# Kernel optimization log

Measured on AMD Instinct MI355X. Metric: run time of the kernel, lower is better.

Reference implementation:

```python
import jax, jax.numpy as jnp
import numpy as np

N_EMBD = 1024
N_HEAD = 16

def _lin_params(key, fan_in, fan_out):
    kw, kb = jax.random.split(key)
    bound = 1.0 / np.sqrt(fan_in)
    W = jax.random.uniform(kw, (fan_in, fan_out), minval=-bound, maxval=bound, dtype=jnp.float32)
    b = jax.random.uniform(kb, (fan_out,), minval=-bound, maxval=bound, dtype=jnp.float32)
    return W, b

def setup_inputs() -> dict:
    key = jax.random.key(0)
    ks = jax.random.split(key, 6)
    x = jax.random.normal(ks[0], (2, 2048, N_EMBD), dtype=jnp.float32)
    W_attn, b_attn = _lin_params(ks[1], N_EMBD, 3 * N_EMBD)
    W_proj, b_proj = _lin_params(ks[2], N_EMBD, N_EMBD)
    W_fc, b_fc = _lin_params(ks[3], N_EMBD, 4 * N_EMBD)
    W_fc2, b_fc2 = _lin_params(ks[4], 4 * N_EMBD, N_EMBD)
    ln1_g = jnp.ones((N_EMBD,), jnp.float32); ln1_b = jnp.zeros((N_EMBD,), jnp.float32)
    ln2_g = jnp.ones((N_EMBD,), jnp.float32); ln2_b = jnp.zeros((N_EMBD,), jnp.float32)
    return {"x": x, "W_attn": W_attn, "b_attn": b_attn, "W_proj": W_proj, "b_proj": b_proj,
            "W_fc": W_fc, "b_fc": b_fc, "W_fc2": W_fc2, "b_fc2": b_fc2,
            "ln1_g": ln1_g, "ln1_b": ln1_b, "ln2_g": ln2_g, "ln2_b": ln2_b}

def _layernorm(x, g, b, eps=1e-5):
    mu = jnp.mean(x, axis=-1, keepdims=True)
    var = jnp.var(x, axis=-1, keepdims=True)
    return (x - mu) * jax.lax.rsqrt(var + eps) * g + b

def _attention(x, W_attn, b_attn, W_proj, b_proj):
    B, T, C = x.shape
    hd = C // N_HEAD
    qkv = x @ W_attn + b_attn                      # [B,T,3C]
    q, k, v = jnp.split(qkv, 3, axis=-1)
    # [B,T,C] -> [B,H,T,hd]
    q = q.reshape(B, T, N_HEAD, hd).transpose(0, 2, 1, 3)
    k = k.reshape(B, T, N_HEAD, hd).transpose(0, 2, 1, 3)
    v = v.reshape(B, T, N_HEAD, hd).transpose(0, 2, 1, 3)
    att = jnp.einsum('bhqd,bhkd->bhqk', q, k) * (1.0 / np.sqrt(hd))
    causal = jnp.tril(jnp.ones((T, T), bool))
    att = jnp.where(causal[None, None], att, -jnp.inf)
    att = jax.nn.softmax(att, axis=-1)
    y = jnp.einsum('bhqk,bhkd->bhqd', att, v)      # [B,H,T,hd]
    y = y.transpose(0, 2, 1, 3).reshape(B, T, C)
    return y @ W_proj + b_proj

def _mlp(x, W_fc, b_fc, W_fc2, b_fc2):
    h = jax.nn.gelu(x @ W_fc + b_fc, approximate=False)
    return h @ W_fc2 + b_fc2

def reference(x, W_attn, b_attn, W_proj, b_proj, W_fc, b_fc, W_fc2, b_fc2,
              ln1_g, ln1_b, ln2_g, ln2_b):
    x = x + _attention(_layernorm(x, ln1_g, ln1_b), W_attn, b_attn, W_proj, b_proj)
    x = x + _mlp(_layernorm(x, ln2_g, ln2_b), W_fc, b_fc, W_fc2, b_fc2)
    return x
```

## Files before the change

### kernel.cpp

```cpp
#include <hip/hip_runtime.h>
#include <cstdint>
#include <cstddef>


typedef unsigned short u16;
typedef short bf16x8 __attribute__((ext_vector_type(8)));
typedef float f32x4 __attribute__((ext_vector_type(4)));

#define C_EMBD 1024
#define T_SEQ  2048
#define N_BATCH 2
#define N_HEADS 16
#define HEAD_D 64
#define M_TOK  4096

__device__ __forceinline__ u16 f2b(float f) {
  union { float f; unsigned u; } v; v.f = f;
  unsigned r = (v.u + 0x7fffu + ((v.u >> 16) & 1u)) >> 16;
  return (u16)r;
}
__device__ __forceinline__ float b2f(u16 u) {
  union { unsigned u; float f; } v; v.u = ((unsigned)u) << 16;
  return v.f;
}
__device__ __forceinline__ void load_lds16(const void* g, void* l) {
  __builtin_amdgcn_global_load_lds(
      (const __attribute__((address_space(1))) void*)g,
      (__attribute__((address_space(3))) void*)l, 16, 0, 0);
}
__device__ __forceinline__ float gelu_fast(float x) {
  const float p = x * __builtin_fmaf(0.044715f * x, x, 1.0f);
  const float t = __builtin_amdgcn_exp2f(2.3021859215f * p);
  return x * t * __builtin_amdgcn_rcpf(t + 1.0f);
}

__global__ __launch_bounds__(256) void transpose_cast(
    const float* __restrict__ W, u16* __restrict__ Wt, int K, int N) {
  __shared__ float tile[32][33];
  const int n0 = blockIdx.x * 32, k0 = blockIdx.y * 32;
  const int tx = threadIdx.x & 31, ty = threadIdx.x >> 5;
#pragma unroll
  for (int i = 0; i < 32; i += 8)
    tile[ty + i][tx] = W[(size_t)(k0 + ty + i) * N + n0 + tx];
  __syncthreads();
#pragma unroll
  for (int i = 0; i < 32; i += 8)
    Wt[(size_t)(n0 + ty + i) * K + k0 + tx] = f2b(tile[tx][ty + i]);
}

__global__ __launch_bounds__(256) void ln_cast(
    const float* __restrict__ X, const float* __restrict__ g,
    const float* __restrict__ b, u16* __restrict__ Y) {
  const int row = blockIdx.x;
  const int tid = threadIdx.x;
  const float4 v = ((const float4*)(X + (size_t)row * C_EMBD))[tid];
  float s = v.x + v.y + v.z + v.w;
  float ss = v.x * v.x + v.y * v.y + v.z * v.z + v.w * v.w;
#pragma unroll
  for (int off = 32; off > 0; off >>= 1) {
    s += __shfl_down(s, off, 64);
    ss += __shfl_down(ss, off, 64);
  }
  __shared__ float red[8];
  __shared__ float stats[2];
  const int wave = tid >> 6, lane = tid & 63;
  if (lane == 0) { red[wave] = s; red[4 + wave] = ss; }
  __syncthreads();
  if (tid == 0) {
    float S = red[0] + red[1] + red[2] + red[3];
    float SS = red[4] + red[5] + red[6] + red[7];
    float mu = S * (1.0f / C_EMBD);
    float var = SS * (1.0f / C_EMBD) - mu * mu;
    stats[0] = mu;
    stats[1] = rsqrtf(var + 1e-5f);
  }
  __syncthreads();
  const float mu = stats[0], rs = stats[1];
  const float4 gv = ((const float4*)g)[tid];
  const float4 bv = ((const float4*)b)[tid];
  ushort4 o;
  o.x = f2b((v.x - mu) * rs * gv.x + bv.x);
  o.y = f2b((v.y - mu) * rs * gv.y + bv.y);
  o.z = f2b((v.z - mu) * rs * gv.z + bv.z);
  o.w = f2b((v.w - mu) * rs * gv.w + bv.w);
  ((ushort4*)(Y + (size_t)row * C_EMBD))[tid] = o;
}

enum { EPI_BF16 = 0, EPI_GELU_BF16 = 2, EPI_PART = 3 };

template <int EPI, int SPLIT>
__global__ __launch_bounds__(256) void gemm_bt(
    const u16* __restrict__ A, const u16* __restrict__ Bt,
    const float* __restrict__ bias,
    void* __restrict__ Cout, void* __restrict__ Cout2, int M, int N, int K) {
  __shared__ u16 As[128 * 64];
  __shared__ u16 Bs[128 * 64];
  const int tid = threadIdx.x;
  const int wave = tid >> 6, lane = tid & 63;
  const int quad = lane >> 4, l16 = lane & 15;
  const int sw = l16 & 7;
  const int m0 = blockIdx.y * 128, n0 = blockIdx.x * 128;
  const int wm = (wave >> 1) * 64, wn = (wave & 1) * 64;

  f32x4 acc[4][4] = {};

  const int kTiles = (K >> 6) / SPLIT;
  const int kt0 = (SPLIT == 2) ? (int)blockIdx.z * kTiles : 0;
  for (int kt = kt0; kt < kt0 + kTiles; ++kt) {
    const int k0 = kt << 6;
#pragma unroll
    for (int i = 0; i < 4; ++i) {
      const int c = tid + i * 256;
      const int row = c >> 3, gc = ((c & 7) ^ (row & 7)) * 8;
      load_lds16(A + (size_t)(m0 + row) * K + k0 + gc, &As[c * 8]);
    }
#pragma unroll
    for (int i = 0; i < 4; ++i) {
      const int c = tid + i * 256;
      const int row = c >> 3, gc = ((c & 7) ^ (row & 7)) * 8;
      load_lds16(Bt + (size_t)(n0 + row) * K + k0 + gc, &Bs[c * 8]);
    }
    __syncthreads();
#pragma unroll
    for (int ks = 0; ks < 2; ++ks) {
      bf16x8 aF[4], bF[4];
#pragma unroll
      for (int t = 0; t < 4; ++t) {
        aF[t] = *(const bf16x8*)
            &As[(wm + t * 16 + l16) * 64 + (((ks * 4 + quad) ^ sw) * 8)];
        bF[t] = *(const bf16x8*)
            &Bs[(wn + t * 16 + l16) * 64 + (((ks * 4 + quad) ^ sw) * 8)];
      }
#pragma unroll
      for (int tm = 0; tm < 4; ++tm)
#pragma unroll
        for (int tn = 0; tn < 4; ++tn)
          acc[tm][tn] = __builtin_amdgcn_mfma_f32_16x16x32_bf16(
              bF[tn], aF[tm], acc[tm][tn], 0, 0, 0);
    }
    __syncthreads();
  }

  float* Pz = (float*)((SPLIT == 2 && blockIdx.z == 1) ? Cout2 : Cout);
#pragma unroll
  for (int tm = 0; tm < 4; ++tm) {
    const int row = m0 + wm + tm * 16 + l16;
#pragma unroll
    for (int tn = 0; tn < 4; ++tn) {
      const int col = n0 + wn + tn * 16 + quad * 4;
      if constexpr (EPI == EPI_PART) {
        *(float4*)&Pz[(size_t)row * N + col] = *(float4*)&acc[tm][tn];
      } else {
        const float4 bz = *(const float4*)&bias[col];
        float v0 = acc[tm][tn][0] + bz.x, v1 = acc[tm][tn][1] + bz.y;
        float v2 = acc[tm][tn][2] + bz.z, v3 = acc[tm][tn][3] + bz.w;
        if constexpr (EPI == EPI_GELU_BF16) {
          v0 = gelu_fast(v0); v1 = gelu_fast(v1);
          v2 = gelu_fast(v2); v3 = gelu_fast(v3);
        }
        ushort4 o;
        o.x = f2b(v0); o.y = f2b(v1); o.z = f2b(v2); o.w = f2b(v3);
        *(ushort4*)&((u16*)Cout)[(size_t)row * N + col] = o;
      }
    }
  }
}

__global__ __launch_bounds__(256) void reduce_add(
    const float* __restrict__ P0, const float* __restrict__ P1,
    const float* __restrict__ bias, const float* __restrict__ res,
    float* __restrict__ out) {
  const int idx = blockIdx.x * 256 + threadIdx.x;
  const float4 a = ((const float4*)P0)[idx];
  const float4 b = ((const float4*)P1)[idx];
  const float4 c = ((const float4*)res)[idx];
  const float4 g = ((const float4*)bias)[idx & 255];
  float4 o;
  o.x = a.x + b.x + c.x + g.x;
  o.y = a.y + b.y + c.y + g.y;
  o.z = a.z + b.z + c.z + g.z;
  o.w = a.w + b.w + c.w + g.w;
  ((float4*)out)[idx] = o;
}

#define Q_SCALE 0.18033688011112042f

__global__ __launch_bounds__(256) void reorder_qkv(
    const u16* __restrict__ qkv, u16* __restrict__ Q, u16* __restrict__ Kb,
    u16* __restrict__ Vt) {
  const int bh = blockIdx.y, tb = blockIdx.x;
  const int b = bh >> 4, h = bh & 15;
  const size_t row0 = (size_t)b * T_SEQ + tb * 64;
  __shared__ u16 vt[64][68];
  const int tid = threadIdx.x;
#pragma unroll
  for (int i = 0; i < 4; ++i) {
    const int e = tid + i * 256;
    const int row = e >> 4, c4 = (e & 15) * 4;
    const u16* src = qkv + (row0 + row) * (3 * C_EMBD) + h * HEAD_D;
    ushort4 qv = *(const ushort4*)(src + c4);
    ushort4 qo;
    qo.x = f2b(b2f(qv.x) * Q_SCALE);
    qo.y = f2b(b2f(qv.y) * Q_SCALE);
    qo.z = f2b(b2f(qv.z) * Q_SCALE);
    qo.w = f2b(b2f(qv.w) * Q_SCALE);
    const size_t dst = ((size_t)bh * T_SEQ + tb * 64 + row) * HEAD_D + c4;
    *(ushort4*)(Q + dst) = qo;
    *(ushort4*)(Kb + dst) = *(const ushort4*)(src + C_EMBD + c4);
    ushort4 vv = *(const ushort4*)(src + 2 * C_EMBD + c4);
    vt[row][c4] = vv.x; vt[row][c4 + 1] = vv.y;
    vt[row][c4 + 2] = vv.z; vt[row][c4 + 3] = vv.w;
  }
  __syncthreads();
#pragma unroll
  for (int i = 0; i < 4; ++i) {
    const int e = tid + i * 256;
    const int d = e >> 4, t4 = (e & 15) * 4;
    ushort4 ov;
    ov.x = vt[t4][d]; ov.y = vt[t4 + 1][d];
    ov.z = vt[t4 + 2][d]; ov.w = vt[t4 + 3][d];
    *(ushort4*)(Vt + ((size_t)bh * HEAD_D + d) * T_SEQ + tb * 64 + t4) = ov;
  }
}

__global__ __launch_bounds__(256) void attn_fwd(
    const u16* __restrict__ Q, const u16* __restrict__ Kb,
    const u16* __restrict__ Vt, u16* __restrict__ Y) {
  const int bh = blockIdx.y;
  const int pair = blockIdx.x;
  const int nqt = (int)(T_SEQ / 64);
  const int tid = threadIdx.x;
  const int wave = tid >> 6, lane = tid & 63;
  const int quad = lane >> 4, l16 = lane & 15;
  const int sw = l16 & 7;
  const u16* Qp = Q + (size_t)bh * T_SEQ * HEAD_D;
  const u16* Kp = Kb + (size_t)bh * T_SEQ * HEAD_D;
  const u16* Vp = Vt + (size_t)bh * HEAD_D * T_SEQ;

  __shared__ u16 Ks[2][64 * 64];
  __shared__ u16 Vs[2][64 * 64];
  __shared__ u16 Pl[4][16 * 72];

  auto stage = [&](u16* dst, const u16* srcBase, size_t stride) {
#pragma unroll
    for (int i = 0; i < 2; ++i) {
      const int c = tid + i * 256;
      const int row = c >> 3;
      const int gc = (c & 7) ^ (row & 7);
      load_lds16(srcBase + (size_t)row * stride + gc * 8, dst + c * 8);
    }
  };

  const int b = bh >> 4, h = bh & 15;

#pragma unroll 1
  for (int phase = 0; phase < 2; ++phase) {
    const int qb = phase == 0 ? (nqt - 1 - pair) : pair;
    const int q0 = qb * 64;
    const int qglob = q0 + wave * 16 + l16;

    if (phase == 1) __syncthreads();

    bf16x8 qF[2];
    qF[0] = *(const bf16x8*)&Qp[(size_t)qglob * HEAD_D + quad * 8];
    qF[1] = *(const bf16x8*)&Qp[(size_t)qglob * HEAD_D + 32 + quad * 8];

    f32x4 o[4] = {};
    float mrun = -3e38f, lrun = 0.0f;

    stage(Ks[0], Kp, HEAD_D);
    stage(Vs[0], Vp, T_SEQ);

    int buf = 0;
    for (int kb = 0; kb <= qb; ++kb) {
      const int k0 = kb * 64;
      __syncthreads();
      if (kb < qb) {
        const int k1 = k0 + 64;
        stage(Ks[buf ^ 1], Kp + (size_t)k1 * HEAD_D, HEAD_D);
        stage(Vs[buf ^ 1], Vp + k1, T_SEQ);
      }
      f32x4 st[4] = {};
#pragma unroll
      for (int ks = 0; ks < 2; ++ks) {
#pragma unroll
        for (int nt = 0; nt < 4; ++nt) {
          bf16x8 kF = *(const bf16x8*)
              &Ks[buf][(nt * 16 + l16) * 64 + (((ks * 4 + quad) ^ sw) * 8)];
          st[nt] = __builtin_amdgcn_mfma_f32_16x16x32_bf16(kF, qF[ks], st[nt],
                                                           0, 0, 0);
        }
      }
      if (kb == qb) {
#pragma unroll
        for (int nt = 0; nt < 4; ++nt) {
#pragma unroll
          for (int r = 0; r < 4; ++r) {
            const int key = k0 + nt * 16 + quad * 4 + r;
            if (key > qglob) st[nt][r] = -3e38f;
          }
        }
      }
      float m = st[0][0];
#pragma unroll
      for (int nt = 0; nt < 4; ++nt)
#pragma unroll
        for (int r = 0; r < 4; ++r) m = fmaxf(m, st[nt][r]);
      m = fmaxf(m, __shfl_xor(m, 16, 64));
      m = fmaxf(m, __shfl_xor(m, 32, 64));
      const float nm = fmaxf(mrun, m);
      const float alpha = __builtin_amdgcn_exp2f(mrun - nm);
      mrun = nm;
      float sum = 0.0f;
#pragma unroll
      for (int nt = 0; nt < 4; ++nt)
#pragma unroll
        for (int r = 0; r < 4; ++r) {
          const float p = __builtin_amdgcn_exp2f(st[nt][r] - nm);
          st[nt][r] = p;
          sum += p;
        }
      sum += __shfl_xor(sum, 16, 64);
      sum += __shfl_xor(sum, 32, 64);
      lrun = lrun * alpha + sum;
#pragma unroll
      for (int nt = 0; nt < 4; ++nt)
#pragma unroll
        for (int r = 0; r < 4; ++r) o[nt][r] *= alpha;
#pragma unroll
      for (int nt = 0; nt < 4; ++nt) {
        ushort4 pk;
        pk.x = f2b(st[nt][0]); pk.y = f2b(st[nt][1]);
        pk.z = f2b(st[nt][2]); pk.w = f2b(st[nt][3]);
        *(ushort4*)&Pl[wave][l16 * 72 + nt * 16 + quad * 4] = pk;
      }
#pragma unroll
      for (int ks = 0; ks < 2; ++ks) {
        bf16x8 aP = *(const bf16x8*)&Pl[wave][l16 * 72 + ks * 32 + quad * 8];
#pragma unroll
        for (int nt = 0; nt < 4; ++nt) {
          bf16x8 vF = *(const bf16x8*)
              &Vs[buf][(nt * 16 + l16) * 64 + (((ks * 4 + quad) ^ sw) * 8)];
          o[nt] =
              __builtin_amdgcn_mfma_f32_16x16x32_bf16(vF, aP, o[nt], 0, 0, 0);
        }
      }
      buf ^= 1;
    }

    const float rl = 1.0f / lrun;
    u16* yp = Y + ((size_t)(b * T_SEQ + qglob)) * C_EMBD + h * HEAD_D;
#pragma unroll
    for (int nt = 0; nt < 4; ++nt) {
      ushort4 ov;
      ov.x = f2b(o[nt][0] * rl); ov.y = f2b(o[nt][1] * rl);
      ov.z = f2b(o[nt][2] * rl); ov.w = f2b(o[nt][3] * rl);
      *(ushort4*)&yp[nt * 16 + quad * 4] = ov;
    }
  }
}

extern "C" void kernel_launch(void* const* d_in, const int* in_sizes, int n_in,
                              void* d_out, int out_size, void* d_ws,
                              size_t ws_size, hipStream_t stream) {
  const float* x      = (const float*)d_in[0];
  const float* W_attn = (const float*)d_in[1];
  const float* b_attn = (const float*)d_in[2];
  const float* W_proj = (const float*)d_in[3];
  const float* b_proj = (const float*)d_in[4];
  const float* W_fc   = (const float*)d_in[5];
  const float* b_fc   = (const float*)d_in[6];
  const float* W_fc2  = (const float*)d_in[7];
  const float* b_fc2  = (const float*)d_in[8];
  const float* ln1_g  = (const float*)d_in[9];
  const float* ln1_b  = (const float*)d_in[10];
  const float* ln2_g  = (const float*)d_in[11];
  const float* ln2_b  = (const float*)d_in[12];

  u16* wqkvT = (u16*)d_ws;
  u16* wprojT = wqkvT + (size_t)3072 * 1024;
  u16* wfcT  = wprojT + (size_t)1024 * 1024;
  u16* wfc2T = wfcT + (size_t)4096 * 1024;
  u16* Abuf  = wfc2T + (size_t)1024 * 4096;
  float* x1  = (float*)(Abuf + (size_t)M_TOK * C_EMBD);
  u16* hbuf  = (u16*)(x1 + (size_t)M_TOK * C_EMBD);
  u16* qkvb  = hbuf;
  float* projP = (float*)hbuf;
  u16* Qb    = hbuf + (size_t)M_TOK * 4096;
  u16* Kbuf  = Qb + (size_t)32 * T_SEQ * HEAD_D;
  u16* Vtb   = Kbuf + (size_t)32 * T_SEQ * HEAD_D;
  float* fc2P1 = (float*)Qb;

  const dim3 blk(256);

  transpose_cast<<<dim3(3072 / 32, 1024 / 32), blk, 0, stream>>>(W_attn, wqkvT, 1024, 3072);
  transpose_cast<<<dim3(1024 / 32, 1024 / 32), blk, 0, stream>>>(W_proj, wprojT, 1024, 1024);
  transpose_cast<<<dim3(4096 / 32, 1024 / 32), blk, 0, stream>>>(W_fc, wfcT, 1024, 4096);
  transpose_cast<<<dim3(1024 / 32, 4096 / 32), blk, 0, stream>>>(W_fc2, wfc2T, 4096, 1024);

  ln_cast<<<M_TOK, blk, 0, stream>>>(x, ln1_g, ln1_b, Abuf);

  gemm_bt<EPI_BF16, 1><<<dim3(3072 / 128, M_TOK / 128), blk, 0, stream>>>(
      Abuf, wqkvT, b_attn, qkvb, nullptr, M_TOK, 3072, 1024);

  reorder_qkv<<<dim3(T_SEQ / 64, 32), blk, 0, stream>>>(qkvb, Qb, Kbuf, Vtb);

  attn_fwd<<<dim3(T_SEQ / 128, 32), blk, 0, stream>>>(Qb, Kbuf, Vtb, Abuf);

  gemm_bt<EPI_PART, 2><<<dim3(1024 / 128, M_TOK / 128, 2), blk, 0, stream>>>(
      Abuf, wprojT, nullptr, projP, projP + (size_t)M_TOK * C_EMBD,
      M_TOK, 1024, 1024);
  reduce_add<<<M_TOK * C_EMBD / 1024, blk, 0, stream>>>(
      projP, projP + (size_t)M_TOK * C_EMBD, b_proj, x, x1);

  ln_cast<<<M_TOK, blk, 0, stream>>>(x1, ln2_g, ln2_b, Abuf);

  gemm_bt<EPI_GELU_BF16, 1><<<dim3(4096 / 128, M_TOK / 128), blk, 0, stream>>>(
      Abuf, wfcT, b_fc, hbuf, nullptr, M_TOK, 4096, 1024);

  gemm_bt<EPI_PART, 2><<<dim3(1024 / 128, M_TOK / 128, 2), blk, 0, stream>>>(
      hbuf, wfc2T, nullptr, d_out, fc2P1, M_TOK, 1024, 4096);
  reduce_add<<<M_TOK * C_EMBD / 1024, blk, 0, stream>>>(
      (const float*)d_out, fc2P1, b_fc2, x1, (float*)d_out);
}
```

Baseline: 375.4 us.

## Fuse QKV head reorder into GEMM epilogue and streamline attention staging

The QKV GEMM epilogue now scales Q and writes Q, K and transposed V straight into per-head layouts, which removes the separate reorder kernel and its round trip through a bf16 qkv buffer. The V-transpose writes become scattered 2-byte stores with a T_SEQ stride, so they are uncoalesced. The attention kernel precomputes its LDS staging offsets and destination pointers. It also packs P to bf16 with a byte permute that truncates instead of rounding to nearest.

Result: faster. 362.2 us (-3.5%).

```diff
diff --git a/kernel.cpp b/kernel.cpp
--- a/kernel.cpp
+++ b/kernel.cpp
@@ -13,6 +13,7 @@
 #define N_HEADS 16
 #define HEAD_D 64
 #define M_TOK  4096
+#define Q_SCALE 0.18033688011112042f
 
 __device__ __forceinline__ u16 f2b(float f) {
   union { float f; unsigned u; } v; v.f = f;
@@ -22,6 +23,10 @@
 __device__ __forceinline__ float b2f(u16 u) {
   union { unsigned u; float f; } v; v.u = ((unsigned)u) << 16;
   return v.f;
+}
+__device__ __forceinline__ unsigned pk2(float a, float b) {
+  union { float f; unsigned u; } x, y; x.f = a; y.f = b;
+  return __builtin_amdgcn_perm(y.u, x.u, 0x07060302u);
 }
 __device__ __forceinline__ void load_lds16(const void* g, void* l) {
   __builtin_amdgcn_global_load_lds(
@@ -86,13 +91,14 @@
   ((ushort4*)(Y + (size_t)row * C_EMBD))[tid] = o;
 }
 
-enum { EPI_BF16 = 0, EPI_GELU_BF16 = 2, EPI_PART = 3 };
+enum { EPI_BF16 = 0, EPI_GELU_BF16 = 2, EPI_PART = 3, EPI_QKV = 4 };
 
 template <int EPI, int SPLIT>
 __global__ __launch_bounds__(256) void gemm_bt(
     const u16* __restrict__ A, const u16* __restrict__ Bt,
     const float* __restrict__ bias,
-    void* __restrict__ Cout, void* __restrict__ Cout2, int M, int N, int K) {
+    void* __restrict__ Cout, void* __restrict__ Cout2, void* __restrict__ Cout3,
+    int M, int N, int K) {
   __shared__ u16 As[128 * 64];
   __shared__ u16 Bs[128 * 64];
   const int tid = threadIdx.x;
@@ -150,6 +156,28 @@
       const int col = n0 + wn + tn * 16 + quad * 4;
       if constexpr (EPI == EPI_PART) {
         *(float4*)&Pz[(size_t)row * N + col] = *(float4*)&acc[tm][tn];
+      } else if constexpr (EPI == EPI_QKV) {
+        const int bb = row >> 11, t = row & (T_SEQ - 1);
+        const float4 bz = *(const float4*)&bias[col];
+        float v0 = acc[tm][tn][0] + bz.x, v1 = acc[tm][tn][1] + bz.y;
+        float v2 = acc[tm][tn][2] + bz.z, v3 = acc[tm][tn][3] + bz.w;
+        const int sec = col >> 10;
+        const int h = (col & 1023) >> 6, d4 = col & 63;
+        const int bh = bb * N_HEADS + h;
+        if (sec == 0) {
+          ushort4 o;
+          o.x = f2b(v0 * Q_SCALE); o.y = f2b(v1 * Q_SCALE);
+          o.z = f2b(v2 * Q_SCALE); o.w = f2b(v3 * Q_SCALE);
+          *(ushort4*)&((u16*)Cout)[((size_t)bh * T_SEQ + t) * HEAD_D + d4] = o;
+        } else if (sec == 1) {
+          ushort4 o;
+          o.x = f2b(v0); o.y = f2b(v1); o.z = f2b(v2); o.w = f2b(v3);
+          *(ushort4*)&((u16*)Cout2)[((size_t)bh * T_SEQ + t) * HEAD_D + d4] = o;
+        } else {
+          u16* vp = (u16*)Cout3 + ((size_t)bh * HEAD_D + d4) * T_SEQ + t;
+          vp[0] = f2b(v0); vp[T_SEQ] = f2b(v1);
+          vp[2 * T_SEQ] = f2b(v2); vp[3 * T_SEQ] = f2b(v3);
+        }
       } else {
         const float4 bz = *(const float4*)&bias[col];
         float v0 = acc[tm][tn][0] + bz.x, v1 = acc[tm][tn][1] + bz.y;
@@ -183,46 +211,6 @@
   ((float4*)out)[idx] = o;
 }
 
-#define Q_SCALE 0.18033688011112042f
-
-__global__ __launch_bounds__(256) void reorder_qkv(
-    const u16* __restrict__ qkv, u16* __restrict__ Q, u16* __restrict__ Kb,
-    u16* __restrict__ Vt) {
-  const int bh = blockIdx.y, tb = blockIdx.x;
-  const int b = bh >> 4, h = bh & 15;
-  const size_t row0 = (size_t)b * T_SEQ + tb * 64;
-  __shared__ u16 vt[64][68];
-  const int tid = threadIdx.x;
-#pragma unroll
-  for (int i = 0; i < 4; ++i) {
-    const int e = tid + i * 256;
-    const int row = e >> 4, c4 = (e & 15) * 4;
-    const u16* src = qkv + (row0 + row) * (3 * C_EMBD) + h * HEAD_D;
-    ushort4 qv = *(const ushort4*)(src + c4);
-    ushort4 qo;
-    qo.x = f2b(b2f(qv.x) * Q_SCALE);
-    qo.y = f2b(b2f(qv.y) * Q_SCALE);
-    qo.z = f2b(b2f(qv.z) * Q_SCALE);
-    qo.w = f2b(b2f(qv.w) * Q_SCALE);
-    const size_t dst = ((size_t)bh * T_SEQ + tb * 64 + row) * HEAD_D + c4;
-    *(ushort4*)(Q + dst) = qo;
-    *(ushort4*)(Kb + dst) = *(const ushort4*)(src + C_EMBD + c4);
-    ushort4 vv = *(const ushort4*)(src + 2 * C_EMBD + c4);
-    vt[row][c4] = vv.x; vt[row][c4 + 1] = vv.y;
-    vt[row][c4 + 2] = vv.z; vt[row][c4 + 3] = vv.w;
-  }
-  __syncthreads();
-#pragma unroll
-  for (int i = 0; i < 4; ++i) {
-    const int e = tid + i * 256;
-    const int d = e >> 4, t4 = (e & 15) * 4;
-    ushort4 ov;
-    ov.x = vt[t4][d]; ov.y = vt[t4 + 1][d];
-    ov.z = vt[t4 + 2][d]; ov.w = vt[t4 + 3][d];
-    *(ushort4*)(Vt + ((size_t)bh * HEAD_D + d) * T_SEQ + tb * 64 + t4) = ov;
-  }
-}
-
 __global__ __launch_bounds__(256) void attn_fwd(
     const u16* __restrict__ Q, const u16* __restrict__ Kb,
     const u16* __restrict__ Vt, u16* __restrict__ Y) {
@@ -241,14 +229,25 @@
   __shared__ u16 Vs[2][64 * 64];
   __shared__ u16 Pl[4][16 * 72];
 
-  auto stage = [&](u16* dst, const u16* srcBase, size_t stride) {
-#pragma unroll
-    for (int i = 0; i < 2; ++i) {
-      const int c = tid + i * 256;
-      const int row = c >> 3;
-      const int gc = (c & 7) ^ (row & 7);
-      load_lds16(srcBase + (size_t)row * stride + gc * 8, dst + c * 8);
-    }
+  const int c1 = tid, c2 = tid + 256;
+  const int r1 = c1 >> 3, g1 = ((c1 & 7) ^ (r1 & 7)) * 8;
+  const int r2 = c2 >> 3, g2 = ((c2 & 7) ^ (r2 & 7)) * 8;
+  const size_t kO1 = (size_t)r1 * HEAD_D + g1, kO2 = (size_t)r2 * HEAD_D + g2;
+  const size_t vO1 = (size_t)r1 * T_SEQ + g1, vO2 = (size_t)r2 * T_SEQ + g2;
+  u16* const dK1[2] = {&Ks[0][c1 * 8], &Ks[1][c1 * 8]};
+  u16* const dK2[2] = {&Ks[0][c2 * 8], &Ks[1][c2 * 8]};
+  u16* const dV1[2] = {&Vs[0][c1 * 8], &Vs[1][c1 * 8]};
+  u16* const dV2[2] = {&Vs[0][c2 * 8], &Vs[1][c2 * 8]};
+
+  auto stageK = [&](int bb, int k0) {
+    const u16* base = Kp + (size_t)k0 * HEAD_D;
+    load_lds16(base + kO1, dK1[bb]);
+    load_lds16(base + kO2, dK2[bb]);
+  };
+  auto stageV = [&](int bb, int k0) {
+    const u16* base = Vp + k0;
+    load_lds16(base + vO1, dV1[bb]);
+    load_lds16(base + vO2, dV2[bb]);
   };
 
   const int b = bh >> 4, h = bh & 15;
@@ -268,17 +267,16 @@
     f32x4 o[4] = {};
     float mrun = -3e38f, lrun = 0.0f;
 
-    stage(Ks[0], Kp, HEAD_D);
-    stage(Vs[0], Vp, T_SEQ);
+    stageK(0, 0);
+    stageV(0, 0);
 
     int buf = 0;
     for (int kb = 0; kb <= qb; ++kb) {
       const int k0 = kb * 64;
       __syncthreads();
       if (kb < qb) {
-        const int k1 = k0 + 64;
-        stage(Ks[buf ^ 1], Kp + (size_t)k1 * HEAD_D, HEAD_D);
-        stage(Vs[buf ^ 1], Vp + k1, T_SEQ);
+        stageK(buf ^ 1, k0 + 64);
+        stageV(buf ^ 1, k0 + 64);
       }
       f32x4 st[4] = {};
 #pragma unroll
@@ -329,10 +327,10 @@
         for (int r = 0; r < 4; ++r) o[nt][r] *= alpha;
 #pragma unroll
       for (int nt = 0; nt < 4; ++nt) {
-        ushort4 pk;
-        pk.x = f2b(st[nt][0]); pk.y = f2b(st[nt][1]);
-        pk.z = f2b(st[nt][2]); pk.w = f2b(st[nt][3]);
-        *(ushort4*)&Pl[wave][l16 * 72 + nt * 16 + quad * 4] = pk;
+        uint2 pk;
+        pk.x = pk2(st[nt][0], st[nt][1]);
+        pk.y = pk2(st[nt][2], st[nt][3]);
+        *(uint2*)&Pl[wave][l16 * 72 + nt * 16 + quad * 4] = pk;
       }
 #pragma unroll
       for (int ks = 0; ks < 2; ++ks) {
@@ -384,7 +382,6 @@
   u16* Abuf  = wfc2T + (size_t)1024 * 4096;
   float* x1  = (float*)(Abuf + (size_t)M_TOK * C_EMBD);
   u16* hbuf  = (u16*)(x1 + (size_t)M_TOK * C_EMBD);
-  u16* qkvb  = hbuf;
   float* projP = (float*)hbuf;
   u16* Qb    = hbuf + (size_t)M_TOK * 4096;
   u16* Kbuf  = Qb + (size_t)32 * T_SEQ * HEAD_D;
@@ -400,15 +397,13 @@
 
   ln_cast<<<M_TOK, blk, 0, stream>>>(x, ln1_g, ln1_b, Abuf);
 
-  gemm_bt<EPI_BF16, 1><<<dim3(3072 / 128, M_TOK / 128), blk, 0, stream>>>(
-      Abuf, wqkvT, b_attn, qkvb, nullptr, M_TOK, 3072, 1024);
-
-  reorder_qkv<<<dim3(T_SEQ / 64, 32), blk, 0, stream>>>(qkvb, Qb, Kbuf, Vtb);
+  gemm_bt<EPI_QKV, 1><<<dim3(3072 / 128, M_TOK / 128), blk, 0, stream>>>(
+      Abuf, wqkvT, b_attn, Qb, Kbuf, Vtb, M_TOK, 3072, 1024);
 
   attn_fwd<<<dim3(T_SEQ / 128, 32), blk, 0, stream>>>(Qb, Kbuf, Vtb, Abuf);
 
   gemm_bt<EPI_PART, 2><<<dim3(1024 / 128, M_TOK / 128, 2), blk, 0, stream>>>(
-      Abuf, wprojT, nullptr, projP, projP + (size_t)M_TOK * C_EMBD,
+      Abuf, wprojT, nullptr, projP, projP + (size_t)M_TOK * C_EMBD, nullptr,
       M_TOK, 1024, 1024);
   reduce_add<<<M_TOK * C_EMBD / 1024, blk, 0, stream>>>(
       projP, projP + (size_t)M_TOK * C_EMBD, b_proj, x, x1);
@@ -416,10 +411,10 @@
   ln_cast<<<M_TOK, blk, 0, stream>>>(x1, ln2_g, ln2_b, Abuf);
 
   gemm_bt<EPI_GELU_BF16, 1><<<dim3(4096 / 128, M_TOK / 128), blk, 0, stream>>>(
-      Abuf, wfcT, b_fc, hbuf, nullptr, M_TOK, 4096, 1024);
+      Abuf, wfcT, b_fc, hbuf, nullptr, nullptr, M_TOK, 4096, 1024);
 
   gemm_bt<EPI_PART, 2><<<dim3(1024 / 128, M_TOK / 128, 2), blk, 0, stream>>>(
-      hbuf, wfc2T, nullptr, d_out, fc2P1, M_TOK, 1024, 4096);
+      hbuf, wfc2T, nullptr, d_out, fc2P1, nullptr, M_TOK, 1024, 4096);
   reduce_add<<<M_TOK * C_EMBD / 1024, blk, 0, stream>>>(
       (const float*)d_out, fc2P1, b_fc2, x1, (float*)d_out);
 }
```
